# Optimization experiments

Hardware: AMD Instinct MI355X
Metric: run time of the kernel (lower is better)

## Reference

```python
import jax, jax.numpy as jnp
import numpy as np

B, T, D = 4, 2048, 1024


def ste_sign(x):
    # forward: sign(x); backward: identity (straight-through)
    return jax.lax.stop_gradient(jnp.sign(x) - x) + x


def setup_inputs() -> dict:
    key = jax.random.key(0)
    kx, kq, kk, kv = jax.random.split(key, 4)
    return {
        "x": jax.random.normal(kx, (B, T, D), dtype=jnp.float32),
        "bv_q": jax.random.normal(kq, (D,), dtype=jnp.float32) * 0.02,
        "bv_k": jax.random.normal(kk, (D,), dtype=jnp.float32) * 0.02,
        "bv_v": jax.random.normal(kv, (D,), dtype=jnp.float32) * 0.02,
    }


def reference(x, bv_q, bv_k, bv_v):
    d = x.shape[-1]
    scale = d ** (-0.5)
    bq = ste_sign(bv_q)
    bk = ste_sign(bv_k)
    bv = ste_sign(bv_v)
    Q = ste_sign(x * bq)          # [B,T,D], values in {-1,0,1}
    K = ste_sign(x * bk)
    V = x * bv                    # [B,T,D]
    scores = jnp.einsum('btd,bsd->bts', Q, K) * scale  # [B,T,T]
    t = x.shape[1]
    causal = jnp.tril(jnp.ones((t, t), dtype=bool))    # [T,T]
    scores = jnp.where(causal, scores, -jnp.inf)
    attn = jax.nn.sigmoid(scores * 4.0)
    attn = jnp.where(causal, attn, 0.0)
    return jnp.einsum('bts,bsd->btd', attn, V)
```

## Files before the change

### kernel.cpp

```cpp
#include <hip/hip_runtime.h>
#include <hip/hip_bf16.h>
#include <stdint.h>
#include <math.h>

#define B_SZ 4
#define T_SZ 2048
#define D_SZ 1024

constexpr int NTH = 512;

typedef short bf16x8 __attribute__((ext_vector_type(8)));
typedef float f32x4 __attribute__((ext_vector_type(4)));
typedef int i32x4 __attribute__((ext_vector_type(4)));
typedef unsigned short ushort8 __attribute__((ext_vector_type(8)));

__device__ __forceinline__ uint32_t sbf(uint32_t xu, uint32_t su) {
  return 0x3F80u | (((xu ^ su) >> 16) & 0x8000u);
}

__device__ __forceinline__ ushort f2bf(float f) {
  uint32_t u = __float_as_uint(f);
  return (ushort)((u + 0x7FFFu + ((u >> 16) & 1u)) >> 16);
}

__device__ __forceinline__ void glds16(const void* g, void* l) {
  __builtin_amdgcn_global_load_lds(
      (const __attribute__((address_space(1))) void*)g,
      (__attribute__((address_space(3))) void*)l, 16, 0, 0);
}


__global__ __launch_bounds__(256) void prep_kernel(
    const float* __restrict__ x, const float* __restrict__ bvq,
    const float* __restrict__ bvk, const float* __restrict__ bvv,
    char* __restrict__ Qb, char* __restrict__ Kb, ushort* __restrict__ Vt2) {
  __shared__ ushort vt[64][72];
  const int bid = blockIdx.x;
  const int dt = bid & 15;
  const int tt = (bid >> 4) & 31;
  const int b = bid >> 9;
  const int t0 = tt * 64, d0 = dt * 64;
  const int tid = threadIdx.x;

#pragma unroll
  for (int p = 0; p < 4; ++p) {
    const int row = p * 16 + (tid >> 4);
    const int c4 = tid & 15;
    const size_t idx = ((size_t)(b * T_SZ + t0 + row)) * D_SZ + d0 + c4 * 4;
    float4 v = *(const float4*)(x + idx);
    float4 q = *(const float4*)(bvq + d0 + c4 * 4);
    float4 k = *(const float4*)(bvk + d0 + c4 * 4);
    float4 s = *(const float4*)(bvv + d0 + c4 * 4);
    uint32_t xu[4] = {__float_as_uint(v.x), __float_as_uint(v.y),
                      __float_as_uint(v.z), __float_as_uint(v.w)};
    uint32_t qu[4] = {__float_as_uint(q.x), __float_as_uint(q.y),
                      __float_as_uint(q.z), __float_as_uint(q.w)};
    uint32_t ku[4] = {__float_as_uint(k.x), __float_as_uint(k.y),
                      __float_as_uint(k.z), __float_as_uint(k.w)};
    uint32_t su[4] = {__float_as_uint(s.x), __float_as_uint(s.y),
                      __float_as_uint(s.z), __float_as_uint(s.w)};
    uint32_t qw = 0, kw = 0;
#pragma unroll
    for (int j = 0; j < 4; ++j) {
      uint32_t qb = ((xu[j] ^ qu[j]) & 0x80000000u) ? 0xFFu : 0x01u;
      uint32_t kb = ((xu[j] ^ ku[j]) & 0x80000000u) ? 0xFFu : 0x01u;
      qw |= qb << (8 * j);
      kw |= kb << (8 * j);
      vt[row][c4 * 4 + j] = f2bf(__uint_as_float(xu[j] ^ (su[j] & 0x80000000u)));
    }
    *(uint32_t*)(Qb + idx) = qw;
    *(uint32_t*)(Kb + idx) = kw;
  }
  __syncthreads();
#pragma unroll
  for (int p = 0; p < 2; ++p) {
    const int dr = p * 32 + (tid >> 3);
    const int tc = tid & 7;
    ushort8 o;
#pragma unroll
    for (int j = 0; j < 8; ++j) o[j] = vt[tc * 8 + j][dr];
    const int dglob = d0 + dr;
    const int s8 = (t0 >> 3) + tc;
    *(ushort8*)(Vt2 +
                (((size_t)(b * 64 + (dglob >> 4))) * 256 + s8) * 128 +
                (dglob & 15) * 8) = o;
  }
}

__global__ __launch_bounds__(NTH) void score_kernel(
    const char* __restrict__ Qb, const char* __restrict__ Kb,
    ushort* __restrict__ P2) {
  __shared__ __align__(16) unsigned char Qs[2][128 * 128];
  __shared__ __align__(16) unsigned char Ks[2][128 * 128];

  const int bid = blockIdx.x;
  const int xcd = bid & 7;
  const int b = xcd >> 1;
  const int j = ((bid >> 3) << 1) + (xcd & 1);
  int qt = (int)((sqrtf(8.f * (float)j + 1.f) - 1.f) * 0.5f);
  while ((qt + 1) * (qt + 2) / 2 <= j) ++qt;
  while (qt * (qt + 1) / 2 > j) --qt;
  const int st = j - qt * (qt + 1) / 2;

  const int tid = threadIdx.x;
  const int lane = tid & 63, w = tid >> 6;
  const int wr = w >> 1, wc = w & 1;
  const int l15 = lane & 15, l4 = lane >> 4;

  const size_t qrow0 = ((size_t)(b * T_SZ + qt * 128)) * D_SZ;
  const size_t krow0 = ((size_t)(b * T_SZ + st * 128)) * D_SZ;

  i32x4 sacc[2][4];
#pragma unroll
  for (int mf = 0; mf < 2; ++mf)
#pragma unroll
    for (int nf = 0; nf < 4; ++nf) sacc[mf][nf] = (i32x4){0, 0, 0, 0};

  auto STAGE = [&](int buf, int ks) {
#pragma unroll
    for (int i = 0; i < 4; ++i) {
      const int isK = i >> 1;
      const int fi = tid + (i & 1) * 512;
      const int row = fi >> 3, c = fi & 7;
      const int cs = c ^ (row & 7);
      const char* src = (isK ? Kb + krow0 : Qb + qrow0) +
                        (size_t)row * D_SZ + ks * 128 + cs * 16;
      unsigned char* dst = (isK ? Ks[buf] : Qs[buf]) + fi * 16;
      glds16(src, dst);
    }
  };

  STAGE(0, 0);
  for (int ks = 0; ks < 8; ++ks) {
    asm volatile("s_waitcnt vmcnt(0)" ::: "memory");
    __builtin_amdgcn_s_barrier();
    if (ks + 1 < 8) STAGE((ks + 1) & 1, ks + 1);
    const int buf = ks & 1;
#pragma unroll
    for (int kc = 0; kc < 2; ++kc) {
      i32x4 af[2], bfr[4];
#pragma unroll
      for (int mf = 0; mf < 2; ++mf) {
        const int row = wr * 32 + mf * 16 + l15;
        const int ch = (kc * 4 + l4) ^ (row & 7);
        af[mf] = *(const i32x4*)(Qs[buf] + row * 128 + ch * 16);
      }
#pragma unroll
      for (int nf = 0; nf < 4; ++nf) {
        const int row = wc * 64 + nf * 16 + l15;
        const int ch = (kc * 4 + l4) ^ (row & 7);
        bfr[nf] = *(const i32x4*)(Ks[buf] + row * 128 + ch * 16);
      }
#pragma unroll
      for (int mf = 0; mf < 2; ++mf)
#pragma unroll
        for (int nf = 0; nf < 4; ++nf)
          sacc[mf][nf] = __builtin_amdgcn_mfma_i32_16x16x64_i8(
              af[mf], bfr[nf], sacc[mf][nf], 0, 0, 0);
    }
    asm volatile("s_waitcnt lgkmcnt(0)" ::: "memory");
  }

#pragma unroll
  for (int mf = 0; mf < 2; ++mf)
#pragma unroll
    for (int nf = 0; nf < 4; ++nf)
#pragma unroll
      for (int r = 0; r < 4; ++r) {
        const int qg = qt * 128 + wr * 32 + mf * 16 + l4 * 4 + r;
        const int sg = st * 128 + wc * 64 + nf * 16 + l15;
        float p = 1.f / (1.f + __expf(-0.125f * (float)sacc[mf][nf][r]));
        if (sg > qg) p = 0.f;
        P2[(((size_t)(b * 128 + (qg >> 4))) * 256 + (sg >> 3)) * 128 +
           (qg & 15) * 8 + (sg & 7)] = f2bf(p);
      }
}

__global__ __launch_bounds__(256) void pv_kernel(
    const ushort* __restrict__ P2, const ushort* __restrict__ Vt2,
    float* __restrict__ out) {
  const int bid = blockIdx.x;
  const int xcd = bid & 7;
  const int k_ = bid >> 3;
  const int g = xcd + 8 * (k_ & 3);
  const int pr = k_ >> 2;
  const int b = g >> 3;
  const int ds = g & 7;

  const int tid = threadIdx.x;
  const int lane = tid & 63, w = tid >> 6;
  const int wr = w >> 1, dg = w & 1;
  const int l15 = lane & 15, l4 = lane >> 4;

  for (int half = 0; half < 2; ++half) {
    const int qt = half ? (31 - pr) : pr;

    f32x4 acc[2][4];
#pragma unroll
    for (int mf = 0; mf < 2; ++mf)
#pragma unroll
      for (int nf = 0; nf < 4; ++nf) acc[mf][nf] = (f32x4){0.f, 0.f, 0.f, 0.f};

    const size_t q4base = (size_t)b * 128 + qt * 4 + wr * 2;
    const size_t d4base = (size_t)b * 64 + ds * 8 + dg * 4;

    for (int st = 0; st <= qt; ++st) {
#pragma unroll
      for (int kk = 0; kk < 2; ++kk) {
        const int s8 = st * 8 + kk * 4 + l4;
        bf16x8 pa[2], vb[4];
#pragma unroll
        for (int mf = 0; mf < 2; ++mf)
          pa[mf] = *(const bf16x8*)(P2 + ((q4base + mf) * 256 + s8) * 128 +
                                    l15 * 8);
#pragma unroll
        for (int nf = 0; nf < 4; ++nf)
          vb[nf] = *(const bf16x8*)(Vt2 + ((d4base + nf) * 256 + s8) * 128 +
                                    l15 * 8);
#pragma unroll
        for (int mf = 0; mf < 2; ++mf)
#pragma unroll
          for (int nf = 0; nf < 4; ++nf)
            acc[mf][nf] = __builtin_amdgcn_mfma_f32_16x16x32_bf16(
                pa[mf], vb[nf], acc[mf][nf], 0, 0, 0);
      }
    }

    float* ob = out + ((size_t)(b * T_SZ + qt * 64 + wr * 32)) * D_SZ +
                ds * 128 + dg * 64;
#pragma unroll
    for (int mf = 0; mf < 2; ++mf)
#pragma unroll
      for (int nf = 0; nf < 4; ++nf)
#pragma unroll
        for (int r = 0; r < 4; ++r)
          ob[(size_t)(mf * 16 + l4 * 4 + r) * D_SZ + nf * 16 + l15] =
              acc[mf][nf][r];
  }
}

__global__ __launch_bounds__(NTH) void hdc_attn_fallback(
    const float* __restrict__ x, const float* __restrict__ bvq,
    const float* __restrict__ bvk, const float* __restrict__ bvv,
    float* __restrict__ out) {
  __shared__ ushort Qs[32][1032];
  __shared__ ushort Ks[64][72];
  __shared__ ushort Ps[32][72];
  const int tid = threadIdx.x;
  const int lane = tid & 63;
  const int w = tid >> 6;
  const int rg = w >> 2, cg = w & 3;
  const int l15 = lane & 15, l4 = lane >> 4;
  const int b = blockIdx.x >> 6;
  const int ti = blockIdx.x & 63;
  const int t0 = ti * 32;
  {
    const float4* xr = (const float4*)(x + ((size_t)b * T_SZ + t0) * D_SZ);
    const float4* bq4 = (const float4*)bvq;
#pragma unroll
    for (int i = 0; i < 16; ++i) {
      int flat4 = tid + i * NTH;
      int row = flat4 >> 8, c4 = flat4 & 255;
      float4 v = xr[row * 256 + c4];
      float4 q = bq4[c4];
      uint32_t q0 = sbf(__float_as_uint(v.x), __float_as_uint(q.x));
      uint32_t q1 = sbf(__float_as_uint(v.y), __float_as_uint(q.y));
      uint32_t q2 = sbf(__float_as_uint(v.z), __float_as_uint(q.z));
      uint32_t q3 = sbf(__float_as_uint(v.w), __float_as_uint(q.w));
      *(uint2*)&Qs[row][c4 * 4] = make_uint2(q0 | (q1 << 16), q2 | (q3 << 16));
    }
  }
  uint32_t vsign[16];
#pragma unroll
  for (int f = 0; f < 16; ++f)
    vsign[f] = __float_as_uint(bvv[cg * 256 + f * 16 + l15]) & 0x80000000u;
  f32x4 acc[16];
#pragma unroll
  for (int f = 0; f < 16; ++f) acc[f] = (f32x4){0.f, 0.f, 0.f, 0.f};
  const int nt = (t0 + 32 + 63) / 64;
  for (int st = 0; st < nt; ++st) {
    const int s0 = st * 64;
    f32x4 sacc = (f32x4){0.f, 0.f, 0.f, 0.f};
    for (int dc = 0; dc < D_SZ / 64; ++dc) {
      __syncthreads();
      {
        const int s = tid >> 3;
        const int c8 = (tid & 7) * 8;
        const float* xk = x + ((size_t)b * T_SZ + s0 + s) * D_SZ + dc * 64 + c8;
        const float* bk = bvk + dc * 64 + c8;
        float4 v0 = *(const float4*)xk;
        float4 v1 = *(const float4*)(xk + 4);
        float4 k0 = *(const float4*)bk;
        float4 k1 = *(const float4*)(bk + 4);
        uint32_t w0 = sbf(__float_as_uint(v0.x), __float_as_uint(k0.x)) |
                      (sbf(__float_as_uint(v0.y), __float_as_uint(k0.y)) << 16);
        uint32_t w1 = sbf(__float_as_uint(v0.z), __float_as_uint(k0.z)) |
                      (sbf(__float_as_uint(v0.w), __float_as_uint(k0.w)) << 16);
        uint32_t w2 = sbf(__float_as_uint(v1.x), __float_as_uint(k1.x)) |
                      (sbf(__float_as_uint(v1.y), __float_as_uint(k1.y)) << 16);
        uint32_t w3 = sbf(__float_as_uint(v1.z), __float_as_uint(k1.z)) |
                      (sbf(__float_as_uint(v1.w), __float_as_uint(k1.w)) << 16);
        *(uint4*)&Ks[s][c8] = make_uint4(w0, w1, w2, w3);
      }
      __syncthreads();
#pragma unroll
      for (int h = 0; h < 2; ++h) {
        bf16x8 a = *(const bf16x8*)&Qs[rg * 16 + l15][dc * 64 + h * 32 + l4 * 8];
        bf16x8 kb = *(const bf16x8*)&Ks[cg * 16 + l15][h * 32 + l4 * 8];
        sacc = __builtin_amdgcn_mfma_f32_16x16x32_bf16(a, kb, sacc, 0, 0, 0);
      }
    }
    {
      const int scol = cg * 16 + l15;
      const int sg = s0 + scol;
#pragma unroll
      for (int r = 0; r < 4; ++r) {
        const int m = rg * 16 + l4 * 4 + r;
        float p = 0.f;
        if (sg <= t0 + m) p = 1.f / (1.f + __expf(-0.125f * sacc[r]));
        Ps[m][scol] = (ushort)(__float_as_uint(p) >> 16);
      }
    }
    __syncthreads();
    const float* xv = x + ((size_t)b * T_SZ + s0) * D_SZ;
#pragma unroll
    for (int kk = 0; kk < 2; ++kk) {
      bf16x8 pa = *(const bf16x8*)&Ps[rg * 16 + l15][kk * 32 + l4 * 8];
      const float* xvs = xv + (size_t)(kk * 32 + l4 * 8) * D_SZ;
#pragma unroll
      for (int f = 0; f < 16; ++f) {
        const int n = cg * 256 + f * 16 + l15;
        const float* xn = xvs + n;
        bf16x8 vb;
#pragma unroll
        for (int i = 0; i < 8; ++i) {
          uint32_t u = __float_as_uint(xn[(size_t)i * D_SZ]) ^ vsign[f];
          vb[i] = (short)(u >> 16);
        }
        acc[f] = __builtin_amdgcn_mfma_f32_16x16x32_bf16(pa, vb, acc[f], 0, 0, 0);
      }
    }
  }
  float* orow = out + ((size_t)b * T_SZ + t0) * D_SZ;
#pragma unroll
  for (int f = 0; f < 16; ++f) {
    const int n = cg * 256 + f * 16 + l15;
#pragma unroll
    for (int r = 0; r < 4; ++r) {
      const int m = rg * 16 + l4 * 4 + r;
      orow[(size_t)m * D_SZ + n] = acc[f][r];
    }
  }
}

extern "C" void kernel_launch(void* const* d_in, const int* in_sizes, int n_in,
                              void* d_out, int out_size, void* d_ws, size_t ws_size,
                              hipStream_t stream) {
  const float* x = (const float*)d_in[0];
  const float* bvq = (const float*)d_in[1];
  const float* bvk = (const float*)d_in[2];
  const float* bvv = (const float*)d_in[3];
  float* out = (float*)d_out;

  const size_t QB_SZ = (size_t)B_SZ * T_SZ * D_SZ;
  const size_t VT_SZ = QB_SZ * 2;
  const size_t P_SZ = (size_t)B_SZ * T_SZ * T_SZ * 2;
  const size_t NEED_FULL = QB_SZ * 2 + VT_SZ + P_SZ;

  if (ws_size >= NEED_FULL) {
    char* Qb = (char*)d_ws;
    char* Kb = Qb + QB_SZ;
    ushort* Vt2 = (ushort*)(Kb + QB_SZ);
    ushort* P2 = (ushort*)((char*)Vt2 + VT_SZ);
    hipLaunchKernelGGL(prep_kernel, dim3(B_SZ * 32 * 16), dim3(256), 0, stream,
                       x, bvq, bvk, bvv, Qb, Kb, Vt2);
    hipLaunchKernelGGL(score_kernel, dim3(544), dim3(NTH), 0, stream,
                       Qb, Kb, P2);
    hipLaunchKernelGGL(pv_kernel, dim3(512), dim3(256), 0, stream,
                       P2, Vt2, out);
  } else {
    hipLaunchKernelGGL(hdc_attn_fallback, dim3(B_SZ * 64), dim3(NTH), 0, stream,
                       x, bvq, bvk, bvv, out);
  }
}
```

Before: 76.97 us.

## Enlarge PV query tile to 128 rows and remap blocks by XCD and batch

The PV kernel now gives each block one 128-row query tile instead of two paired 64-row tiles. Each wave accumulates a 4x4 MFMA fragment grid rather than 2x4, which raises reuse of loaded V fragments per P fragment. Block indices are remapped so each XCD pair serves one batch with alternating query-tile parity, heavy tiles scheduled first, for better L2 locality. The inner loop uses pointer increments with unroll 2. The cost is more accumulator registers and the loss of the previous triangular load-balancing pairing. This relies on the launch grid and the P2 layout matching the new 128-row tiling, which are not visible here.

Result: slower. 78.57 us (+2.1%).

```diff
diff --git a/kernel.cpp b/kernel.cpp
--- a/kernel.cpp
+++ b/kernel.cpp
@@ -181,62 +181,67 @@
     float* __restrict__ out) {
   const int bid = blockIdx.x;
   const int xcd = bid & 7;
-  const int k_ = bid >> 3;
-  const int g = xcd + 8 * (k_ & 3);
-  const int pr = k_ >> 2;
-  const int b = g >> 3;
-  const int ds = g & 7;
+  const int b = xcd >> 1;
+  const int par = xcd & 1;
+  const int t = bid >> 3;
+  const int ds = t & 7;
+  const int qi = 7 - (t >> 3);
+  const int qt = qi * 2 + par;
 
   const int tid = threadIdx.x;
   const int lane = tid & 63, w = tid >> 6;
   const int wr = w >> 1, dg = w & 1;
   const int l15 = lane & 15, l4 = lane >> 4;
 
-  for (int half = 0; half < 2; ++half) {
-    const int qt = half ? (31 - pr) : pr;
-
-    f32x4 acc[2][4];
-#pragma unroll
-    for (int mf = 0; mf < 2; ++mf)
-#pragma unroll
-      for (int nf = 0; nf < 4; ++nf) acc[mf][nf] = (f32x4){0.f, 0.f, 0.f, 0.f};
-
-    const size_t q4base = (size_t)b * 128 + qt * 4 + wr * 2;
-    const size_t d4base = (size_t)b * 64 + ds * 8 + dg * 4;
-
-    for (int st = 0; st <= qt; ++st) {
-#pragma unroll
-      for (int kk = 0; kk < 2; ++kk) {
-        const int s8 = st * 8 + kk * 4 + l4;
-        bf16x8 pa[2], vb[4];
-#pragma unroll
-        for (int mf = 0; mf < 2; ++mf)
-          pa[mf] = *(const bf16x8*)(P2 + ((q4base + mf) * 256 + s8) * 128 +
-                                    l15 * 8);
-#pragma unroll
-        for (int nf = 0; nf < 4; ++nf)
-          vb[nf] = *(const bf16x8*)(Vt2 + ((d4base + nf) * 256 + s8) * 128 +
-                                    l15 * 8);
-#pragma unroll
-        for (int mf = 0; mf < 2; ++mf)
-#pragma unroll
-          for (int nf = 0; nf < 4; ++nf)
-            acc[mf][nf] = __builtin_amdgcn_mfma_f32_16x16x32_bf16(
-                pa[mf], vb[nf], acc[mf][nf], 0, 0, 0);
-      }
-    }
-
-    float* ob = out + ((size_t)(b * T_SZ + qt * 64 + wr * 32)) * D_SZ +
-                ds * 128 + dg * 64;
-#pragma unroll
-    for (int mf = 0; mf < 2; ++mf)
+  f32x4 acc[4][4];
+#pragma unroll
+  for (int mf = 0; mf < 4; ++mf)
+#pragma unroll
+    for (int nf = 0; nf < 4; ++nf) acc[mf][nf] = (f32x4){0.f, 0.f, 0.f, 0.f};
+
+  const size_t q4base = (size_t)b * 128 + qt * 8 + wr * 4;
+  const size_t d4base = (size_t)b * 64 + ds * 8 + dg * 4;
+
+  const ushort* pP[4];
+  const ushort* pV[4];
+#pragma unroll
+  for (int i = 0; i < 4; ++i) {
+    pP[i] = P2 + ((q4base + i) * 256 + l4) * 128 + l15 * 8;
+    pV[i] = Vt2 + ((d4base + i) * 256 + l4) * 128 + l15 * 8;
+  }
+
+  const int nk = qt * 4 + 4;
+#pragma unroll 2
+  for (int k = 0; k < nk; ++k) {
+    bf16x8 pa[4], vb[4];
+#pragma unroll
+    for (int i = 0; i < 4; ++i) {
+      pa[i] = *(const bf16x8*)pP[i];
+      vb[i] = *(const bf16x8*)pV[i];
+    }
+#pragma unroll
+    for (int i = 0; i < 4; ++i) {
+      pP[i] += 512;
+      pV[i] += 512;
+    }
+#pragma unroll
+    for (int mf = 0; mf < 4; ++mf)
 #pragma unroll
       for (int nf = 0; nf < 4; ++nf)
-#pragma unroll
-        for (int r = 0; r < 4; ++r)
-          ob[(size_t)(mf * 16 + l4 * 4 + r) * D_SZ + nf * 16 + l15] =
-              acc[mf][nf][r];
-  }
+        acc[mf][nf] = __builtin_amdgcn_mfma_f32_16x16x32_bf16(
+            pa[mf], vb[nf], acc[mf][nf], 0, 0, 0);
+  }
+
+  float* ob = out + ((size_t)(b * T_SZ + qt * 128 + wr * 64)) * D_SZ +
+              ds * 128 + dg * 64;
+#pragma unroll
+  for (int mf = 0; mf < 4; ++mf)
+#pragma unroll
+    for (int nf = 0; nf < 4; ++nf)
+#pragma unroll
+      for (int r = 0; r < 4; ++r)
+        ob[(size_t)(mf * 16 + l4 * 4 + r) * D_SZ + nf * 16 + l15] =
+            acc[mf][nf][r];
 }
 
 __global__ __launch_bounds__(NTH) void hdc_attn_fallback(
```
